# Optimization experiments

Measured on AMD Instinct MI355X. Metric: run time of the kernel, lower is better.

Reference implementation:

```python
import jax, jax.numpy as jnp
import numpy as np

B, S, D, N, NC = 2, 1024, 1024, 8192, 8


def _srw_chunked(x, h, emb_norm, tau_offset, w_read, w_write, n_chunks):
    Bd, Sd, Dd = x.shape
    Nd = emb_norm.shape[0]
    cs = Nd // n_chunks
    h_bf = h.astype(jnp.bfloat16)
    x_bf = x.astype(jnp.bfloat16)
    emb_bf = emb_norm.astype(jnp.bfloat16)
    read_bf = w_read.astype(jnp.bfloat16)
    write_bf = w_write.astype(jnp.bfloat16)
    z1 = jnp.zeros((Bd, Sd, 1))

    @jax.checkpoint
    def estimate_stats(h, emb, nc_val):
        ec0 = jax.lax.dynamic_slice_in_dim(emb, 0, cs, axis=0)
        sc0 = h @ ec0.T
        s_sum = sc0.sum(axis=-1, keepdims=True).astype(jnp.float32) * nc_val
        sq_sum = (sc0 ** 2).sum(axis=-1, keepdims=True).astype(jnp.float32) * nc_val
        return (s_sum, sq_sum)

    s_sum, sq_sum = estimate_stats(h_bf, emb_bf, n_chunks)
    s_mean = s_sum / Nd
    s_std = jnp.sqrt(sq_sum / Nd - s_mean ** 2) + 1e-08
    tau = s_mean + tau_offset * s_std
    tau_bf = tau.astype(jnp.bfloat16)

    @jax.checkpoint
    def gsrw_step(carry, i):
        out, es, em, ac, lbs, lbq = carry
        s = i * cs
        ec = jax.lax.dynamic_slice_in_dim(emb_bf, s, cs, axis=0)
        rc = jax.lax.dynamic_slice_in_dim(read_bf, s, cs, axis=0)
        wc = jax.lax.dynamic_slice_in_dim(write_bf, s, cs, axis=0)
        sc = h_bf @ ec.T  # [B,S,cs]
        raw = sc - tau_bf
        gc = jnp.where(raw > 0, raw, (1e-06 * jnp.exp(jnp.clip(raw.astype(jnp.float32), -10.0, 0.0))).astype(jnp.bfloat16))
        gc = jnp.clip(gc, 0.0, 10.0)
        eg = (jnp.exp(gc.astype(jnp.float32)) - 1.0).astype(jnp.bfloat16)
        ef = eg.astype(jnp.float32)
        xr = x_bf @ rc.T  # [B,S,cs]
        co = ((eg * xr) @ wc).astype(jnp.float32)  # [B,S,D]
        gn = ef.mean(axis=(0, 1))
        lbs = lbs + gn.sum()
        lbq = lbq + (gn ** 2).sum()
        return ((out + co,
                 es + ef.sum(axis=-1, keepdims=True),
                 jnp.maximum(em, ef.max(axis=-1, keepdims=True)),
                 ac + (raw > 0).sum(axis=-1, keepdims=True).astype(jnp.float32),
                 lbs, lbq), None)

    z_scalar = jnp.float32(0.0)
    init = (jnp.zeros((Bd, Sd, Dd), dtype=jnp.float32), z1,
            jnp.full((Bd, Sd, 1), -1000000000.0), z1, z_scalar, z_scalar)
    (raw_out, tes, tem, tac, lb_sum, lb_sq), _ = jax.lax.scan(gsrw_step, init, jnp.arange(n_chunks))
    inv_es = (1.0 / (tes + 1e-08)).astype(jnp.bfloat16)
    gs = jnp.tanh(tem).astype(jnp.bfloat16)
    out = raw_out * inv_es * gs
    exp_sum_scalar = tes.mean() + 1e-08
    norm_lb_sum = lb_sum / exp_sum_scalar
    norm_lb_sq = lb_sq / exp_sum_scalar ** 2
    lb_loss = norm_lb_sq * Nd - 2.0 * norm_lb_sum + 1.0
    gs_mean = jnp.tanh(tem).mean()
    es_mean = tes.mean()
    return (out.astype(jnp.float32), tac / Nd, tem, lb_loss, gs_mean, es_mean)


def setup_inputs() -> dict:
    key = jax.random.key(0)
    k = jax.random.split(key, 6)
    x = jax.random.normal(k[0], (B, S, D), jnp.float32)
    h = jax.random.normal(k[1], (B, S, D), jnp.float32)
    emb = jax.random.normal(k[2], (N, D), jnp.float32) * 0.02
    w_read = jax.random.normal(k[3], (N, D), jnp.float32) * 0.02
    w_write = jax.random.normal(k[4], (N, D), jnp.float32) * 0.02
    tau_offset = jax.random.normal(k[5], (B, S, 1), jnp.float32) * 0.1
    return {"x": x, "h": h, "emb": emb, "tau_offset": tau_offset,
            "w_read": w_read, "w_write": w_write, "n_chunks": NC}


def reference(x, h, emb, tau_offset, w_read, w_write, n_chunks):
    # caller (_know_forward) unit-normalizes the embedding pool first
    emb_norm = emb / (jnp.linalg.norm(emb, axis=-1, keepdims=True) + 1e-08)
    out, active_frac, gate_max, lb_loss, gs_mean, es_mean = _srw_chunked(
        x, h, emb_norm, tau_offset, w_read, w_write, n_chunks)
    return out
```

## Files before the change

kernel.cpp:

```cpp
#include <hip/hip_runtime.h>


#define MDIM 2048
#define DDIM 1024
#define NDIM 8192

typedef __attribute__((ext_vector_type(8))) __bf16 bf16x8;
typedef __attribute__((ext_vector_type(4))) float f32x4;

static __device__ __forceinline__ unsigned short f2b(float f) {
  unsigned u = __float_as_uint(f);
  u = (u + 0x7FFFu + ((u >> 16) & 1u)) >> 16;
  return (unsigned short)u;
}
static __device__ __forceinline__ float b2f(unsigned short s) {
  return __uint_as_float(((unsigned)s) << 16);
}

#define LDSF(off) (*(const bf16x8*)(lds + (off)))
#define MFMA_BF16 __builtin_amdgcn_mfma_f32_16x16x32_bf16

static __device__ __forceinline__ void stage_half(const unsigned short* __restrict__ src,
                                                  int ld, int row0, int k0,
                                                  char* lds, int lds_off, int w, int l) {
  const int rsub = l >> 3;
  const int col = k0 + 8 * ((l & 7) ^ rsub);
#pragma unroll
  for (int j = 0; j < 2; ++j) {
    const unsigned short* g =
        src + (size_t)(row0 + w * 8 + j * 64 + rsub) * (size_t)ld + col;
    __builtin_amdgcn_global_load_lds(
        (const __attribute__((address_space(1))) unsigned int*)(const void*)g,
        (__attribute__((address_space(3))) unsigned int*)(void*)(lds + lds_off + j * 8192 + w * 1024),
        16, 0, 0);
  }
}

template <int PAR, bool SA, bool SB, int VMC>
static __device__ __forceinline__ void ktile(const unsigned short* __restrict__ asrc,
                                             const unsigned short* __restrict__ bsrc,
                                             int ld, int m0, int n0, int kA, int kB,
                                             char* lds, f32x4 (&acc)[8][4],
                                             int w, int l, int wr, int wc,
                                             int arow_off, int brow_off, int kx0, int kx1) {
  const int ab = PAR * 65536 + wr * 16384;
  const int bb = PAR * 65536 + 32768 + (wc >> 1) * 16384;
  const int nxt = (1 - PAR) * 65536;
  bf16x8 a[4][2], blo[2][2], bhi[2][2];
  if (SA) stage_half(asrc, ld, m0, kA, lds, nxt, w, l);
#pragma unroll
  for (int m = 0; m < 4; ++m) {
    a[m][0] = LDSF(ab + arow_off + m * 2048 + kx0);
    a[m][1] = LDSF(ab + arow_off + m * 2048 + kx1);
  }
#pragma unroll
  for (int n = 0; n < 2; ++n) {
    blo[n][0] = LDSF(bb + brow_off + n * 2048 + kx0);
    blo[n][1] = LDSF(bb + brow_off + n * 2048 + kx1);
  }
  asm volatile("s_waitcnt lgkmcnt(8)" ::: "memory");
  __builtin_amdgcn_s_barrier();
  asm volatile("s_waitcnt lgkmcnt(0)" ::: "memory");
  __builtin_amdgcn_s_setprio(1);
#pragma unroll
  for (int ks = 0; ks < 2; ++ks)
#pragma unroll
    for (int n = 0; n < 2; ++n)
#pragma unroll
      for (int m = 0; m < 4; ++m)
        acc[m][n] = MFMA_BF16(a[m][ks], blo[n][ks], acc[m][n], 0, 0, 0);
  __builtin_amdgcn_s_setprio(0);
  __builtin_amdgcn_s_barrier();
  if (SA) stage_half(asrc, ld, m0 + 128, kA, lds, nxt + 16384, w, l);
#pragma unroll
  for (int n = 0; n < 2; ++n) {
    bhi[n][0] = LDSF(bb + brow_off + (n + 2) * 2048 + kx0);
    bhi[n][1] = LDSF(bb + brow_off + (n + 2) * 2048 + kx1);
  }
  __builtin_amdgcn_s_barrier();
  asm volatile("s_waitcnt lgkmcnt(0)" ::: "memory");
  __builtin_amdgcn_s_setprio(1);
#pragma unroll
  for (int ks = 0; ks < 2; ++ks)
#pragma unroll
    for (int n = 0; n < 2; ++n)
#pragma unroll
      for (int m = 0; m < 4; ++m)
        acc[m][n + 2] = MFMA_BF16(a[m][ks], bhi[n][ks], acc[m][n + 2], 0, 0, 0);
  __builtin_amdgcn_s_setprio(0);
  __builtin_amdgcn_s_barrier();
  if (SB) stage_half(bsrc, ld, n0, kB, lds, PAR * 65536 + 32768, w, l);
#pragma unroll
  for (int m = 0; m < 4; ++m) {
    a[m][0] = LDSF(ab + arow_off + (m + 4) * 2048 + kx0);
    a[m][1] = LDSF(ab + arow_off + (m + 4) * 2048 + kx1);
  }
  __builtin_amdgcn_s_barrier();
  asm volatile("s_waitcnt lgkmcnt(0)" ::: "memory");
  __builtin_amdgcn_s_setprio(1);
#pragma unroll
  for (int ks = 0; ks < 2; ++ks)
#pragma unroll
    for (int n = 0; n < 2; ++n)
#pragma unroll
      for (int m = 0; m < 4; ++m)
        acc[m + 4][n + 2] = MFMA_BF16(a[m][ks], bhi[n][ks], acc[m + 4][n + 2], 0, 0, 0);
  __builtin_amdgcn_s_setprio(0);
  __builtin_amdgcn_s_barrier();
  if (SB) stage_half(bsrc, ld, n0 + 128, kB, lds, PAR * 65536 + 49152, w, l);
  __builtin_amdgcn_s_setprio(1);
#pragma unroll
  for (int ks = 0; ks < 2; ++ks)
#pragma unroll
    for (int n = 0; n < 2; ++n)
#pragma unroll
      for (int m = 0; m < 4; ++m)
        acc[m + 4][n] = MFMA_BF16(a[m][ks], blo[n][ks], acc[m + 4][n], 0, 0, 0);
  __builtin_amdgcn_s_setprio(0);
  if (VMC == 4) asm volatile("s_waitcnt vmcnt(4)" ::: "memory");
  if (VMC == 0) asm volatile("s_waitcnt vmcnt(0)" ::: "memory");
  __builtin_amdgcn_s_barrier();
}

static __device__ __forceinline__ void gemm256(const unsigned short* __restrict__ asrc,
                                               const unsigned short* __restrict__ bsrc,
                                               int ld, int m0, int n0, int kbase,
                                               char* lds, f32x4 (&acc)[8][4],
                                               int w, int l, int wr, int wc) {
  const int lrow = l & 15, lk = l >> 4;
  const int axor = (l & 7) << 4;
  const int kx0 = (lk << 4) ^ axor;
  const int kx1 = (64 | (lk << 4)) ^ axor;
  const int arow_off = lrow * 128;
  const int brow_off = ((wc & 1) * 64 + lrow) * 128;

  stage_half(asrc, ld, m0,       kbase,      lds, 0,             w, l);
  stage_half(asrc, ld, m0 + 128, kbase,      lds, 16384,         w, l);
  stage_half(bsrc, ld, n0,       kbase,      lds, 32768,         w, l);
  stage_half(bsrc, ld, n0 + 128, kbase,      lds, 49152,         w, l);
  stage_half(bsrc, ld, n0,       kbase + 64, lds, 65536 + 32768, w, l);
  stage_half(bsrc, ld, n0 + 128, kbase + 64, lds, 65536 + 49152, w, l);
  asm volatile("s_waitcnt vmcnt(4)" ::: "memory");
  __builtin_amdgcn_s_barrier();

#pragma unroll 1
  for (int s = 0; s < 14; s += 2) {
    ktile<0, true, true, 4>(asrc, bsrc, ld, m0, n0, kbase + (s + 1) * 64,
                            kbase + (s + 2) * 64, lds, acc, w, l, wr, wc,
                            arow_off, brow_off, kx0, kx1);
    ktile<1, true, true, 4>(asrc, bsrc, ld, m0, n0, kbase + (s + 2) * 64,
                            kbase + (s + 3) * 64, lds, acc, w, l, wr, wc,
                            arow_off, brow_off, kx0, kx1);
  }
  ktile<0, true, false, 0>(asrc, bsrc, ld, m0, n0, kbase + 15 * 64, 0, lds, acc,
                           w, l, wr, wc, arow_off, brow_off, kx0, kx1);
  ktile<1, false, false, -1>(asrc, bsrc, ld, m0, n0, 0, 0, lds, acc,
                             w, l, wr, wc, arow_off, brow_off, kx0, kx1);
}


__global__ __launch_bounds__(256) void k_prep(const float* __restrict__ emb,
                                              const float* __restrict__ w_read,
                                              const float* __restrict__ h,
                                              const float* __restrict__ x,
                                              const float* __restrict__ w_write,
                                              unsigned short* __restrict__ eb,
                                              unsigned short* __restrict__ rb,
                                              unsigned short* __restrict__ hb,
                                              unsigned short* __restrict__ xb,
                                              unsigned short* __restrict__ wbT) {
  const int b = blockIdx.x, t = threadIdx.x;
  if (b < 8192) {
    const float4 v = ((const float4*)(emb + (size_t)b * 1024))[t];
    float ss = v.x * v.x + v.y * v.y + v.z * v.z + v.w * v.w;
#pragma unroll
    for (int off = 1; off < 64; off <<= 1) ss += __shfl_xor(ss, off, 64);
    __shared__ float wsum[4];
    if ((t & 63) == 0) wsum[t >> 6] = ss;
    __syncthreads();
    const float denom = sqrtf(wsum[0] + wsum[1] + wsum[2] + wsum[3]) + 1e-8f;
    ushort4 o;
    o.x = f2b(v.x / denom);
    o.y = f2b(v.y / denom);
    o.z = f2b(v.z / denom);
    o.w = f2b(v.w / denom);
    ((ushort4*)(eb + (size_t)b * 1024))[t] = o;
  } else if (b < 20480) {
    const float* src;
    unsigned short* dst;
    int i;
    if (b < 16384) { src = w_read; dst = rb; i = (b - 8192) * 256 + t; }
    else if (b < 18432) { src = h; dst = hb; i = (b - 16384) * 256 + t; }
    else { src = x; dst = xb; i = (b - 18432) * 256 + t; }
    const float4 v = ((const float4*)src)[i];
    ushort4 o;
    o.x = f2b(v.x);
    o.y = f2b(v.y);
    o.z = f2b(v.z);
    o.w = f2b(v.w);
    ((ushort4*)dst)[i] = o;
  } else {
    __shared__ float tsm[64][65];
    const int b2 = b - 20480;
    const int nb = b2 & 127, db = b2 >> 7;
    const int r = t >> 2, c4 = (t & 3) * 16;
#pragma unroll
    for (int j = 0; j < 4; ++j) {
      const float4 v = *(const float4*)&w_write[(size_t)(nb * 64 + r) * 1024 + db * 64 + c4 + 4 * j];
      tsm[r][c4 + 4 * j + 0] = v.x;
      tsm[r][c4 + 4 * j + 1] = v.y;
      tsm[r][c4 + 4 * j + 2] = v.z;
      tsm[r][c4 + 4 * j + 3] = v.w;
    }
    __syncthreads();
    const int dr = t >> 2, nc0 = (t & 3) * 16;
    unsigned pk[8];
#pragma unroll
    for (int j = 0; j < 8; ++j) {
      const unsigned lo = f2b(tsm[nc0 + 2 * j][dr]);
      const unsigned hi = f2b(tsm[nc0 + 2 * j + 1][dr]);
      pk[j] = lo | (hi << 16);
    }
    uint4* dst = (uint4*)(wbT + (size_t)(db * 64 + dr) * 8192 + nb * 64 + nc0);
    uint4 w0, w1;
    w0.x = pk[0]; w0.y = pk[1]; w0.z = pk[2]; w0.w = pk[3];
    w1.x = pk[4]; w1.y = pk[5]; w1.z = pk[6]; w1.w = pk[7];
    dst[0] = w0;
    dst[1] = w1;
  }
}


template <int TROWS>
static __device__ __forceinline__ void stage_tile(const unsigned short* __restrict__ src,
                                                  int row0, int k0, int ld,
                                                  unsigned short* lds, int wave, int lane) {
  const int rsub = lane >> 3;
  const int csub = (lane & 7) << 3;
#pragma unroll
  for (int q = 0; q < TROWS / 32; ++q) {
    const int p = q * 4 + wave;
    const unsigned short* g =
        src + (size_t)(row0 + p * 8 + rsub) * (size_t)ld + (size_t)(k0 + csub);
    __builtin_amdgcn_global_load_lds(
        (const __attribute__((address_space(1))) unsigned int*)(const void*)g,
        (__attribute__((address_space(3))) unsigned int*)(void*)(lds + p * 512),
        16, 0, 0);
  }
}

__global__ __launch_bounds__(256, 2) void k_stats(const unsigned short* __restrict__ hb,
                                                  const unsigned short* __restrict__ eb,
                                                  float* __restrict__ stat_s,
                                                  float* __restrict__ stat_q) {
  __shared__ unsigned short a_sm[128 * 64];
  __shared__ unsigned short b_sm[128 * 64];
  __shared__ float red_s[2][128];
  __shared__ float red_q[2][128];
  const int t = threadIdx.x;
  const int wave = t >> 6, lane = t & 63;
  const int wr = wave >> 1, wc = wave & 1;
  const int m0 = blockIdx.x * 128, n0 = blockIdx.y * 128;
  const int arow = lane & 15;
  const int kcol = (lane >> 4) << 3;
  f32x4 acc[4][4];
#pragma unroll
  for (int m = 0; m < 4; ++m)
#pragma unroll
    for (int n = 0; n < 4; ++n) acc[m][n] = (f32x4)0.0f;
  for (int k0 = 0; k0 < 1024; k0 += 64) {
    stage_tile<128>(hb, m0, k0, 1024, a_sm, wave, lane);
    stage_tile<128>(eb, n0, k0, 1024, b_sm, wave, lane);
    asm volatile("s_waitcnt vmcnt(0)" ::: "memory");
    __syncthreads();
#pragma unroll
    for (int ks = 0; ks < 2; ++ks) {
      bf16x8 af[4], bfr[4];
#pragma unroll
      for (int m = 0; m < 4; ++m)
        af[m] = *(const bf16x8*)&a_sm[(wr * 64 + m * 16 + arow) * 64 + ks * 32 + kcol];
#pragma unroll
      for (int n = 0; n < 4; ++n)
        bfr[n] = *(const bf16x8*)&b_sm[(wc * 64 + n * 16 + arow) * 64 + ks * 32 + kcol];
#pragma unroll
      for (int m = 0; m < 4; ++m)
#pragma unroll
        for (int n = 0; n < 4; ++n)
          acc[m][n] = MFMA_BF16(af[m], bfr[n], acc[m][n], 0, 0, 0);
    }
    __syncthreads();
  }

  float s_r[4][4], q_r[4][4];
#pragma unroll
  for (int m = 0; m < 4; ++m)
#pragma unroll
    for (int i = 0; i < 4; ++i) { s_r[m][i] = 0.f; q_r[m][i] = 0.f; }
#pragma unroll
  for (int m = 0; m < 4; ++m)
#pragma unroll
    for (int n = 0; n < 4; ++n)
#pragma unroll
      for (int i = 0; i < 4; ++i) {
        const float scf = b2f(f2b(acc[m][n][i]));
        s_r[m][i] += scf;
        q_r[m][i] += b2f(f2b(scf * scf));
      }
#pragma unroll
  for (int m = 0; m < 4; ++m)
#pragma unroll
    for (int i = 0; i < 4; ++i) {
      float s = s_r[m][i], q = q_r[m][i];
      for (int off = 1; off < 16; off <<= 1) {
        s += __shfl_xor(s, off, 64);
        q += __shfl_xor(q, off, 64);
      }
      if ((lane & 15) == 0) {
        const int rloc = wr * 64 + m * 16 + (lane >> 4) * 4 + i;
        red_s[wc][rloc] = s;
        red_q[wc][rloc] = q;
      }
    }
  __syncthreads();
  if (t < 128) {
    stat_s[(size_t)(m0 + t) * 8 + blockIdx.y] = red_s[0][t] + red_s[1][t];
    stat_q[(size_t)(m0 + t) * 8 + blockIdx.y] = red_q[0][t] + red_q[1][t];
  }
}

__global__ void k_tau(const float* __restrict__ stat_s, const float* __restrict__ stat_q,
                      const float* __restrict__ tau_off, float* __restrict__ tau) {
  const int r = blockIdx.x * 256 + threadIdx.x;
  if (r >= MDIM) return;
  float S = 0.f, Q = 0.f;
#pragma unroll
  for (int j = 0; j < 8; ++j) {
    S += stat_s[(size_t)r * 8 + j];
    Q += stat_q[(size_t)r * 8 + j];
  }
  const float s_sum = S * 8.0f;
  const float sq_sum = Q * 8.0f;
  const float mean = s_sum * (1.0f / 8192.0f);
  const float var = __fsub_rn(sq_sum * (1.0f / 8192.0f), __fmul_rn(mean, mean));
  const float sd = __fadd_rn(__fsqrt_rn(var), 1e-8f);
  const float tv = __fadd_rn(mean, __fmul_rn(tau_off[r], sd));
  tau[r] = b2f(f2b(tv));
}


__global__ __launch_bounds__(512, 2) void k_gate(const unsigned short* __restrict__ hb,
                                                 const unsigned short* __restrict__ eb,
                                                 const unsigned short* __restrict__ xb,
                                                 const unsigned short* __restrict__ rb,
                                                 const float* __restrict__ tau,
                                                 unsigned short* __restrict__ Aeg,
                                                 float* __restrict__ es_part,
                                                 float* __restrict__ em_part) {
  __shared__ __align__(16) char lds[131072];
  const int t = threadIdx.x, w = t >> 6, l = t & 63;
  const int wr = w >> 2, wc = w & 3;
  const int bid = blockIdx.x;
  const int swz = (bid & 7) * 32 + (bid >> 3);
  const int m0 = (swz >> 5) * 256, n0 = (swz & 31) * 256;
  const int lrow = l & 15, lk = l >> 4;

  f32x4 acc[8][4];
#pragma unroll
  for (int m = 0; m < 8; ++m)
#pragma unroll
    for (int n = 0; n < 4; ++n) acc[m][n] = (f32x4)0.0f;
  gemm256(hb, eb, 1024, m0, n0, 0, lds, acc, w, l, wr, wc);

  __syncthreads();
  float* tau_sm = (float*)lds;
  float* red_es = (float*)(lds + 1024);
  float* red_em = (float*)(lds + 1024 + 4096);
  if (t < 256) tau_sm[t] = tau[m0 + t];
  __syncthreads();
#pragma unroll
  for (int m = 0; m < 8; ++m) {
#pragma unroll
    for (int i = 0; i < 4; ++i) {
      const int rl = wr * 128 + m * 16 + lk * 4 + i;
      const float taub = tau_sm[rl];
      float es_v = 0.f, em_v = 0.f;
#pragma unroll
      for (int n = 0; n < 4; ++n) {
        const float scf = b2f(f2b(acc[m][n][i]));
        const float rawf = b2f(f2b(scf - taub));
        float gcf;
        if (rawf > 0.f) gcf = fminf(rawf, 10.0f);
        else gcf = b2f(f2b(1e-6f * expf(fmaxf(rawf, -10.0f))));
        const unsigned short egu = f2b(expf(gcf) - 1.0f);
        const float ef = b2f(egu);
        es_v += ef;
        em_v = fmaxf(em_v, ef);
        Aeg[(size_t)(m0 + rl) * NDIM + (size_t)(n0 + wc * 64 + n * 16 + lrow)] = egu;
      }
      for (int off = 1; off < 16; off <<= 1) {
        es_v += __shfl_xor(es_v, off, 64);
        em_v = fmaxf(em_v, __shfl_xor(em_v, off, 64));
      }
      if (lrow == 0) {
        red_es[wc * 256 + rl] = es_v;
        red_em[wc * 256 + rl] = em_v;
      }
    }
  }
  __syncthreads();
  if (t < 256) {
    const float s = red_es[t] + red_es[256 + t] + red_es[512 + t] + red_es[768 + t];
    const float e = fmaxf(fmaxf(red_em[t], red_em[256 + t]),
                          fmaxf(red_em[512 + t], red_em[768 + t]));
    es_part[(size_t)(m0 + t) * 32 + (n0 >> 8)] = s;
    em_part[(size_t)(m0 + t) * 32 + (n0 >> 8)] = e;
  }
  __syncthreads();

#pragma unroll
  for (int m = 0; m < 8; ++m)
#pragma unroll
    for (int n = 0; n < 4; ++n) acc[m][n] = (f32x4)0.0f;
  gemm256(xb, rb, 1024, m0, n0, 0, lds, acc, w, l, wr, wc);

#pragma unroll
  for (int m = 0; m < 8; ++m)
#pragma unroll
    for (int n = 0; n < 4; ++n)
#pragma unroll
      for (int i = 0; i < 4; ++i) {
        const int rl = wr * 128 + m * 16 + lk * 4 + i;
        const size_t idx =
            (size_t)(m0 + rl) * NDIM + (size_t)(n0 + wc * 64 + n * 16 + lrow);
        const unsigned short egu = Aeg[idx];
        const float xrf = b2f(f2b(acc[m][n][i]));
        Aeg[idx] = f2b(b2f(egu) * xrf);
      }
}


__global__ __launch_bounds__(512, 2) void k_out(const unsigned short* __restrict__ A,
                                                const unsigned short* __restrict__ wbT,
                                                unsigned short* __restrict__ pacc) {
  __shared__ __align__(16) char lds[131072];
  const int t = threadIdx.x, w = t >> 6, l = t & 63;
  const int wr = w >> 2, wc = w & 3;
  const int bid = blockIdx.x;
  const int swz = (bid & 7) * 32 + (bid >> 3);
  const int bm = swz >> 5, chunk = (swz >> 2) & 7, bd = swz & 3;
  const int m0 = bm * 256, d0 = bd * 256;
  f32x4 acc[8][4];
#pragma unroll
  for (int m = 0; m < 8; ++m)
#pragma unroll
    for (int n = 0; n < 4; ++n) acc[m][n] = (f32x4)0.0f;
  gemm256(A, wbT, 8192, m0, d0, chunk * 1024, lds, acc, w, l, wr, wc);

  const int lrow = l & 15, lk = l >> 4;
#pragma unroll
  for (int m = 0; m < 8; ++m)
#pragma unroll
    for (int n = 0; n < 4; ++n)
#pragma unroll
      for (int i = 0; i < 4; ++i) {
        const int rl = wr * 128 + m * 16 + lk * 4 + i;
        pacc[((size_t)chunk * MDIM + (m0 + rl)) * DDIM +
             (size_t)(d0 + wc * 64 + n * 16 + lrow)] = f2b(acc[m][n][i]);
      }
}


__global__ void k_scale(const float* __restrict__ es_part, const float* __restrict__ em_part,
                        float* __restrict__ scale2) {
  const int r = blockIdx.x * 256 + threadIdx.x;
  if (r >= MDIM) return;
  float s = 0.f, m = 0.f;
#pragma unroll
  for (int j = 0; j < 32; ++j) {
    s += es_part[(size_t)r * 32 + j];
    m = fmaxf(m, em_part[(size_t)r * 32 + j]);
  }
  scale2[2 * r] = b2f(f2b(1.0f / (s + 1e-8f)));
  scale2[2 * r + 1] = b2f(f2b(tanhf(m)));
}

__global__ __launch_bounds__(256) void k_finish(const unsigned short* __restrict__ pacc,
                                                const float* __restrict__ scale2,
                                                float* __restrict__ outp) {
  const int t = blockIdx.x * 256 + threadIdx.x;
  const int r = t >> 8;
  const int d4 = (t & 255) * 4;
  float sx = 0.f, sy = 0.f, sz = 0.f, sw = 0.f;
#pragma unroll
  for (int c = 0; c < 8; ++c) {
    const ushort4 v = *(const ushort4*)(pacc + ((size_t)c * MDIM + r) * DDIM + d4);
    sx += b2f(v.x);
    sy += b2f(v.y);
    sz += b2f(v.z);
    sw += b2f(v.w);
  }
  const float inv = scale2[2 * r];
  const float gsv = scale2[2 * r + 1];
  float4 o;
  o.x = (sx * inv) * gsv;
  o.y = (sy * inv) * gsv;
  o.z = (sz * inv) * gsv;
  o.w = (sw * inv) * gsv;
  *(float4*)(outp + (size_t)r * DDIM + d4) = o;
}


extern "C" void kernel_launch(void* const* d_in, const int* in_sizes, int n_in,
                              void* d_out, int out_size, void* d_ws, size_t ws_size,
                              hipStream_t stream) {
  const float* x = (const float*)d_in[0];
  const float* h = (const float*)d_in[1];
  const float* emb = (const float*)d_in[2];
  const float* tau_off = (const float*)d_in[3];
  const float* w_read = (const float*)d_in[4];
  const float* w_write = (const float*)d_in[5];

  char* ws = (char*)d_ws;
  const size_t MB = 1024 * 1024;
  unsigned short* rb = (unsigned short*)(ws);
  unsigned short* eb = (unsigned short*)(ws + 16 * MB);
  unsigned short* wbT = (unsigned short*)(ws + 32 * MB);
  unsigned short* hb = (unsigned short*)(ws + 48 * MB);
  unsigned short* xb = (unsigned short*)(ws + 52 * MB);
  unsigned short* Aeg = (unsigned short*)(ws + 56 * MB);
  unsigned short* pacc = (unsigned short*)(ws);
  float* tau = (float*)(ws + 88 * MB);
  float* stat_s = (float*)(ws + 88 * MB + 1 * 65536);
  float* stat_q = (float*)(ws + 88 * MB + 2 * 65536);
  float* es_part = (float*)(ws + 88 * MB + 3 * 65536);
  float* em_part = (float*)(ws + 88 * MB + 7 * 65536);
  float* scale2 = (float*)(ws + 88 * MB + 11 * 65536);
  if (ws_size < 88 * MB + 12 * 65536) return;
  float* outp = (float*)d_out;

  k_prep<<<22528, 256, 0, stream>>>(emb, w_read, h, x, w_write, eb, rb, hb, xb, wbT);
  k_stats<<<dim3(MDIM / 128, 8), 256, 0, stream>>>(hb, eb, stat_s, stat_q);
  k_tau<<<MDIM / 256, 256, 0, stream>>>(stat_s, stat_q, tau_off, tau);
  k_gate<<<256, 512, 0, stream>>>(hb, eb, xb, rb, tau, Aeg, es_part, em_part);
  k_scale<<<MDIM / 256, 256, 0, stream>>>(es_part, em_part, scale2);
  k_out<<<256, 512, 0, stream>>>(Aeg, wbT, pacc);
  k_finish<<<(MDIM * DDIM / 4) / 256, 256, 0, stream>>>(pacc, scale2, outp);
}
```

Baseline: 224.9 us.

## Simplify GEMM pipeline, split gate kernel into two, reorder prep blocks

The hand-scheduled ktile pipeline, with its interleaved half-tile staging and many barriers, is replaced by a plain double-buffered loop. Each iteration stages the whole next k-tile, then runs the MFMAs with a single vmcnt wait and one barrier. The fused gate kernel is split into a score/gate kernel and a separate xr kernel, which lowers register pressure per kernel but adds a launch and a round trip of Aeg through memory. The w_write transpose blocks in k_prep now come first, so the heavier blocks are scheduled early.

```diff
diff --git a/kernel.cpp b/kernel.cpp
--- a/kernel.cpp
+++ b/kernel.cpp
@@ -36,90 +36,14 @@
   }
 }
 
-template <int PAR, bool SA, bool SB, int VMC>
-static __device__ __forceinline__ void ktile(const unsigned short* __restrict__ asrc,
-                                             const unsigned short* __restrict__ bsrc,
-                                             int ld, int m0, int n0, int kA, int kB,
-                                             char* lds, f32x4 (&acc)[8][4],
-                                             int w, int l, int wr, int wc,
-                                             int arow_off, int brow_off, int kx0, int kx1) {
-  const int ab = PAR * 65536 + wr * 16384;
-  const int bb = PAR * 65536 + 32768 + (wc >> 1) * 16384;
-  const int nxt = (1 - PAR) * 65536;
-  bf16x8 a[4][2], blo[2][2], bhi[2][2];
-  if (SA) stage_half(asrc, ld, m0, kA, lds, nxt, w, l);
-#pragma unroll
-  for (int m = 0; m < 4; ++m) {
-    a[m][0] = LDSF(ab + arow_off + m * 2048 + kx0);
-    a[m][1] = LDSF(ab + arow_off + m * 2048 + kx1);
-  }
-#pragma unroll
-  for (int n = 0; n < 2; ++n) {
-    blo[n][0] = LDSF(bb + brow_off + n * 2048 + kx0);
-    blo[n][1] = LDSF(bb + brow_off + n * 2048 + kx1);
-  }
-  asm volatile("s_waitcnt lgkmcnt(8)" ::: "memory");
-  __builtin_amdgcn_s_barrier();
-  asm volatile("s_waitcnt lgkmcnt(0)" ::: "memory");
-  __builtin_amdgcn_s_setprio(1);
-#pragma unroll
-  for (int ks = 0; ks < 2; ++ks)
-#pragma unroll
-    for (int n = 0; n < 2; ++n)
-#pragma unroll
-      for (int m = 0; m < 4; ++m)
-        acc[m][n] = MFMA_BF16(a[m][ks], blo[n][ks], acc[m][n], 0, 0, 0);
-  __builtin_amdgcn_s_setprio(0);
-  __builtin_amdgcn_s_barrier();
-  if (SA) stage_half(asrc, ld, m0 + 128, kA, lds, nxt + 16384, w, l);
-#pragma unroll
-  for (int n = 0; n < 2; ++n) {
-    bhi[n][0] = LDSF(bb + brow_off + (n + 2) * 2048 + kx0);
-    bhi[n][1] = LDSF(bb + brow_off + (n + 2) * 2048 + kx1);
-  }
-  __builtin_amdgcn_s_barrier();
-  asm volatile("s_waitcnt lgkmcnt(0)" ::: "memory");
-  __builtin_amdgcn_s_setprio(1);
-#pragma unroll
-  for (int ks = 0; ks < 2; ++ks)
-#pragma unroll
-    for (int n = 0; n < 2; ++n)
-#pragma unroll
-      for (int m = 0; m < 4; ++m)
-        acc[m][n + 2] = MFMA_BF16(a[m][ks], bhi[n][ks], acc[m][n + 2], 0, 0, 0);
-  __builtin_amdgcn_s_setprio(0);
-  __builtin_amdgcn_s_barrier();
-  if (SB) stage_half(bsrc, ld, n0, kB, lds, PAR * 65536 + 32768, w, l);
-#pragma unroll
-  for (int m = 0; m < 4; ++m) {
-    a[m][0] = LDSF(ab + arow_off + (m + 4) * 2048 + kx0);
-    a[m][1] = LDSF(ab + arow_off + (m + 4) * 2048 + kx1);
-  }
-  __builtin_amdgcn_s_barrier();
-  asm volatile("s_waitcnt lgkmcnt(0)" ::: "memory");
-  __builtin_amdgcn_s_setprio(1);
-#pragma unroll
-  for (int ks = 0; ks < 2; ++ks)
-#pragma unroll
-    for (int n = 0; n < 2; ++n)
-#pragma unroll
-      for (int m = 0; m < 4; ++m)
-        acc[m + 4][n + 2] = MFMA_BF16(a[m][ks], bhi[n][ks], acc[m + 4][n + 2], 0, 0, 0);
-  __builtin_amdgcn_s_setprio(0);
-  __builtin_amdgcn_s_barrier();
-  if (SB) stage_half(bsrc, ld, n0 + 128, kB, lds, PAR * 65536 + 49152, w, l);
-  __builtin_amdgcn_s_setprio(1);
-#pragma unroll
-  for (int ks = 0; ks < 2; ++ks)
-#pragma unroll
-    for (int n = 0; n < 2; ++n)
-#pragma unroll
-      for (int m = 0; m < 4; ++m)
-        acc[m + 4][n] = MFMA_BF16(a[m][ks], blo[n][ks], acc[m + 4][n], 0, 0, 0);
-  __builtin_amdgcn_s_setprio(0);
-  if (VMC == 4) asm volatile("s_waitcnt vmcnt(4)" ::: "memory");
-  if (VMC == 0) asm volatile("s_waitcnt vmcnt(0)" ::: "memory");
-  __builtin_amdgcn_s_barrier();
+static __device__ __forceinline__ void stage4(const unsigned short* __restrict__ asrc,
+                                              const unsigned short* __restrict__ bsrc,
+                                              int ld, int m0, int n0, int k0,
+                                              char* lds, int buf, int w, int l) {
+  stage_half(asrc, ld, m0,       k0, lds, buf,         w, l);
+  stage_half(asrc, ld, m0 + 128, k0, lds, buf + 16384, w, l);
+  stage_half(bsrc, ld, n0,       k0, lds, buf + 32768, w, l);
+  stage_half(bsrc, ld, n0 + 128, k0, lds, buf + 49152, w, l);
 }
 
 static __device__ __forceinline__ void gemm256(const unsigned short* __restrict__ asrc,
@@ -134,28 +58,75 @@
   const int arow_off = lrow * 128;
   const int brow_off = ((wc & 1) * 64 + lrow) * 128;
 
-  stage_half(asrc, ld, m0,       kbase,      lds, 0,             w, l);
-  stage_half(asrc, ld, m0 + 128, kbase,      lds, 16384,         w, l);
-  stage_half(bsrc, ld, n0,       kbase,      lds, 32768,         w, l);
-  stage_half(bsrc, ld, n0 + 128, kbase,      lds, 49152,         w, l);
-  stage_half(bsrc, ld, n0,       kbase + 64, lds, 65536 + 32768, w, l);
-  stage_half(bsrc, ld, n0 + 128, kbase + 64, lds, 65536 + 49152, w, l);
-  asm volatile("s_waitcnt vmcnt(4)" ::: "memory");
+  stage4(asrc, bsrc, ld, m0, n0, kbase, lds, 0, w, l);
+  asm volatile("s_waitcnt vmcnt(0)" ::: "memory");
   __builtin_amdgcn_s_barrier();
 
 #pragma unroll 1
-  for (int s = 0; s < 14; s += 2) {
-    ktile<0, true, true, 4>(asrc, bsrc, ld, m0, n0, kbase + (s + 1) * 64,
-                            kbase + (s + 2) * 64, lds, acc, w, l, wr, wc,
-                            arow_off, brow_off, kx0, kx1);
-    ktile<1, true, true, 4>(asrc, bsrc, ld, m0, n0, kbase + (s + 2) * 64,
-                            kbase + (s + 3) * 64, lds, acc, w, l, wr, wc,
-                            arow_off, brow_off, kx0, kx1);
-  }
-  ktile<0, true, false, 0>(asrc, bsrc, ld, m0, n0, kbase + 15 * 64, 0, lds, acc,
-                           w, l, wr, wc, arow_off, brow_off, kx0, kx1);
-  ktile<1, false, false, -1>(asrc, bsrc, ld, m0, n0, 0, 0, lds, acc,
-                             w, l, wr, wc, arow_off, brow_off, kx0, kx1);
+  for (int t = 0; t < 16; ++t) {
+    const int buf = (t & 1) * 65536;
+    const int nbuf = 65536 - buf;
+    if (t < 15) stage4(asrc, bsrc, ld, m0, n0, kbase + (t + 1) * 64, lds, nbuf, w, l);
+
+    const int ab = buf + wr * 16384;
+    const int bb = buf + 32768 + (wc >> 1) * 16384;
+    bf16x8 aLO[4][2], aHI[4][2], bLO[2][2], bHI[2][2];
+#pragma unroll
+    for (int m = 0; m < 4; ++m) {
+      aLO[m][0] = LDSF(ab + arow_off + m * 2048 + kx0);
+      aLO[m][1] = LDSF(ab + arow_off + m * 2048 + kx1);
+    }
+#pragma unroll
+    for (int n = 0; n < 2; ++n) {
+      bLO[n][0] = LDSF(bb + brow_off + n * 2048 + kx0);
+      bLO[n][1] = LDSF(bb + brow_off + n * 2048 + kx1);
+      bHI[n][0] = LDSF(bb + brow_off + (n + 2) * 2048 + kx0);
+      bHI[n][1] = LDSF(bb + brow_off + (n + 2) * 2048 + kx1);
+    }
+    asm volatile("s_waitcnt lgkmcnt(0)" ::: "memory");
+    __builtin_amdgcn_s_setprio(1);
+#pragma unroll
+    for (int ks = 0; ks < 2; ++ks)
+#pragma unroll
+      for (int n = 0; n < 2; ++n)
+#pragma unroll
+        for (int m = 0; m < 4; ++m)
+          acc[m][n] = MFMA_BF16(aLO[m][ks], bLO[n][ks], acc[m][n], 0, 0, 0);
+    __builtin_amdgcn_s_setprio(0);
+#pragma unroll
+    for (int m = 0; m < 4; ++m) {
+      aHI[m][0] = LDSF(ab + arow_off + (m + 4) * 2048 + kx0);
+      aHI[m][1] = LDSF(ab + arow_off + (m + 4) * 2048 + kx1);
+    }
+    __builtin_amdgcn_s_setprio(1);
+#pragma unroll
+    for (int ks = 0; ks < 2; ++ks)
+#pragma unroll
+      for (int n = 0; n < 2; ++n)
+#pragma unroll
+        for (int m = 0; m < 4; ++m)
+          acc[m][n + 2] = MFMA_BF16(aLO[m][ks], bHI[n][ks], acc[m][n + 2], 0, 0, 0);
+    __builtin_amdgcn_s_setprio(0);
+    asm volatile("s_waitcnt lgkmcnt(0)" ::: "memory");
+    __builtin_amdgcn_s_setprio(1);
+#pragma unroll
+    for (int ks = 0; ks < 2; ++ks)
+#pragma unroll
+      for (int n = 0; n < 2; ++n)
+#pragma unroll
+        for (int m = 0; m < 4; ++m)
+          acc[m + 4][n + 2] = MFMA_BF16(aHI[m][ks], bHI[n][ks], acc[m + 4][n + 2], 0, 0, 0);
+#pragma unroll
+    for (int ks = 0; ks < 2; ++ks)
+#pragma unroll
+      for (int n = 0; n < 2; ++n)
+#pragma unroll
+        for (int m = 0; m < 4; ++m)
+          acc[m + 4][n] = MFMA_BF16(aHI[m][ks], bLO[n][ks], acc[m + 4][n], 0, 0, 0);
+    __builtin_amdgcn_s_setprio(0);
+    asm volatile("s_waitcnt vmcnt(0)" ::: "memory");
+    __builtin_amdgcn_s_barrier();
+  }
 }
 
 
@@ -170,8 +141,36 @@
                                               unsigned short* __restrict__ xb,
                                               unsigned short* __restrict__ wbT) {
   const int b = blockIdx.x, t = threadIdx.x;
-  if (b < 8192) {
-    const float4 v = ((const float4*)(emb + (size_t)b * 1024))[t];
+  if (b < 2048) {
+    __shared__ float tsm[64][65];
+    const int nb = b & 127, db = b >> 7;
+    const int r = t >> 2, c4 = (t & 3) * 16;
+#pragma unroll
+    for (int j = 0; j < 4; ++j) {
+      const float4 v = *(const float4*)&w_write[(size_t)(nb * 64 + r) * 1024 + db * 64 + c4 + 4 * j];
+      tsm[r][c4 + 4 * j + 0] = v.x;
+      tsm[r][c4 + 4 * j + 1] = v.y;
+      tsm[r][c4 + 4 * j + 2] = v.z;
+      tsm[r][c4 + 4 * j + 3] = v.w;
+    }
+    __syncthreads();
+    const int dr = t >> 2, nc0 = (t & 3) * 16;
+    unsigned pk[8];
+#pragma unroll
+    for (int j = 0; j < 8; ++j) {
+      const unsigned lo = f2b(tsm[nc0 + 2 * j][dr]);
+      const unsigned hi = f2b(tsm[nc0 + 2 * j + 1][dr]);
+      pk[j] = lo | (hi << 16);
+    }
+    uint4* dst = (uint4*)(wbT + (size_t)(db * 64 + dr) * 8192 + nb * 64 + nc0);
+    uint4 w0, w1;
+    w0.x = pk[0]; w0.y = pk[1]; w0.z = pk[2]; w0.w = pk[3];
+    w1.x = pk[4]; w1.y = pk[5]; w1.z = pk[6]; w1.w = pk[7];
+    dst[0] = w0;
+    dst[1] = w1;
+  } else if (b < 10240) {
+    const int n = b - 2048;
+    const float4 v = ((const float4*)(emb + (size_t)n * 1024))[t];
     float ss = v.x * v.x + v.y * v.y + v.z * v.z + v.w * v.w;
 #pragma unroll
     for (int off = 1; off < 64; off <<= 1) ss += __shfl_xor(ss, off, 64);
@@ -184,14 +183,14 @@
     o.y = f2b(v.y / denom);
     o.z = f2b(v.z / denom);
     o.w = f2b(v.w / denom);
-    ((ushort4*)(eb + (size_t)b * 1024))[t] = o;
-  } else if (b < 20480) {
+    ((ushort4*)(eb + (size_t)n * 1024))[t] = o;
+  } else {
     const float* src;
     unsigned short* dst;
     int i;
-    if (b < 16384) { src = w_read; dst = rb; i = (b - 8192) * 256 + t; }
-    else if (b < 18432) { src = h; dst = hb; i = (b - 16384) * 256 + t; }
-    else { src = x; dst = xb; i = (b - 18432) * 256 + t; }
+    if (b < 18432) { src = w_read; dst = rb; i = (b - 10240) * 256 + t; }
+    else if (b < 20480) { src = h; dst = hb; i = (b - 18432) * 256 + t; }
+    else { src = x; dst = xb; i = (b - 20480) * 256 + t; }
     const float4 v = ((const float4*)src)[i];
     ushort4 o;
     o.x = f2b(v.x);
@@ -199,34 +198,6 @@
     o.z = f2b(v.z);
     o.w = f2b(v.w);
     ((ushort4*)dst)[i] = o;
-  } else {
-    __shared__ float tsm[64][65];
-    const int b2 = b - 20480;
-    const int nb = b2 & 127, db = b2 >> 7;
-    const int r = t >> 2, c4 = (t & 3) * 16;
-#pragma unroll
-    for (int j = 0; j < 4; ++j) {
-      const float4 v = *(const float4*)&w_write[(size_t)(nb * 64 + r) * 1024 + db * 64 + c4 + 4 * j];
-      tsm[r][c4 + 4 * j + 0] = v.x;
-      tsm[r][c4 + 4 * j + 1] = v.y;
-      tsm[r][c4 + 4 * j + 2] = v.z;
-      tsm[r][c4 + 4 * j + 3] = v.w;
-    }
-    __syncthreads();
-    const int dr = t >> 2, nc0 = (t & 3) * 16;
-    unsigned pk[8];
-#pragma unroll
-    for (int j = 0; j < 8; ++j) {
-      const unsigned lo = f2b(tsm[nc0 + 2 * j][dr]);
-      const unsigned hi = f2b(tsm[nc0 + 2 * j + 1][dr]);
-      pk[j] = lo | (hi << 16);
-    }
-    uint4* dst = (uint4*)(wbT + (size_t)(db * 64 + dr) * 8192 + nb * 64 + nc0);
-    uint4 w0, w1;
-    w0.x = pk[0]; w0.y = pk[1]; w0.z = pk[2]; w0.w = pk[3];
-    w1.x = pk[4]; w1.y = pk[5]; w1.z = pk[6]; w1.w = pk[7];
-    dst[0] = w0;
-    dst[1] = w1;
   }
 }
 
@@ -348,22 +319,18 @@
 }
 
 
-__global__ __launch_bounds__(512, 2) void k_gate(const unsigned short* __restrict__ hb,
-                                                 const unsigned short* __restrict__ eb,
-                                                 const unsigned short* __restrict__ xb,
-                                                 const unsigned short* __restrict__ rb,
-                                                 const float* __restrict__ tau,
-                                                 unsigned short* __restrict__ Aeg,
-                                                 float* __restrict__ es_part,
-                                                 float* __restrict__ em_part) {
+__global__ __launch_bounds__(512, 2) void k_sc(const unsigned short* __restrict__ hb,
+                                               const unsigned short* __restrict__ eb,
+                                               const float* __restrict__ tau,
+                                               unsigned short* __restrict__ Aeg,
+                                               float* __restrict__ es_part,
+                                               float* __restrict__ em_part) {
   __shared__ __align__(16) char lds[131072];
   const int t = threadIdx.x, w = t >> 6, l = t & 63;
   const int wr = w >> 2, wc = w & 3;
   const int bid = blockIdx.x;
   const int swz = (bid & 7) * 32 + (bid >> 3);
   const int m0 = (swz >> 5) * 256, n0 = (swz & 31) * 256;
-  const int lrow = l & 15, lk = l >> 4;
-
   f32x4 acc[8][4];
 #pragma unroll
   for (int m = 0; m < 8; ++m)
@@ -377,6 +344,7 @@
   float* red_em = (float*)(lds + 1024 + 4096);
   if (t < 256) tau_sm[t] = tau[m0 + t];
   __syncthreads();
+  const int lrow = l & 15, lk = l >> 4;
 #pragma unroll
   for (int m = 0; m < 8; ++m) {
 #pragma unroll
@@ -415,14 +383,26 @@
     es_part[(size_t)(m0 + t) * 32 + (n0 >> 8)] = s;
     em_part[(size_t)(m0 + t) * 32 + (n0 >> 8)] = e;
   }
-  __syncthreads();
-
+}
+
+
+__global__ __launch_bounds__(512, 2) void k_xr(const unsigned short* __restrict__ xb,
+                                               const unsigned short* __restrict__ rb,
+                                               unsigned short* __restrict__ Aeg) {
+  __shared__ __align__(16) char lds[131072];
+  const int t = threadIdx.x, w = t >> 6, l = t & 63;
+  const int wr = w >> 2, wc = w & 3;
+  const int bid = blockIdx.x;
+  const int swz = (bid & 7) * 32 + (bid >> 3);
+  const int m0 = (swz >> 5) * 256, n0 = (swz & 31) * 256;
+  f32x4 acc[8][4];
 #pragma unroll
   for (int m = 0; m < 8; ++m)
 #pragma unroll
     for (int n = 0; n < 4; ++n) acc[m][n] = (f32x4)0.0f;
   gemm256(xb, rb, 1024, m0, n0, 0, lds, acc, w, l, wr, wc);
 
+  const int lrow = l & 15, lk = l >> 4;
 #pragma unroll
   for (int m = 0; m < 8; ++m)
 #pragma unroll
@@ -541,8 +521,9 @@
   k_prep<<<22528, 256, 0, stream>>>(emb, w_read, h, x, w_write, eb, rb, hb, xb, wbT);
   k_stats<<<dim3(MDIM / 128, 8), 256, 0, stream>>>(hb, eb, stat_s, stat_q);
   k_tau<<<MDIM / 256, 256, 0, stream>>>(stat_s, stat_q, tau_off, tau);
-  k_gate<<<256, 512, 0, stream>>>(hb, eb, xb, rb, tau, Aeg, es_part, em_part);
+  k_sc<<<256, 512, 0, stream>>>(hb, eb, tau, Aeg, es_part, em_part);
   k_scale<<<MDIM / 256, 256, 0, stream>>>(es_part, em_part, scale2);
+  k_xr<<<256, 512, 0, stream>>>(xb, rb, Aeg);
   k_out<<<256, 512, 0, stream>>>(Aeg, wbT, pacc);
   k_finish<<<(MDIM * DDIM / 4) / 256, 256, 0, stream>>>(pacc, scale2, outp);
 }
```

New measurement: 197.1 us. 1.14x faster.
